# Kernel optimization log

Measured on AMD Instinct MI355X. Metric: run time of the kernel, lower is better.

Reference implementation:

```python
import jax, jax.numpy as jnp
import numpy as np

B, T, NB = 8192, 18, 6
EH, DH = 256, 256
NIN = NB + 1  # encoder GRU input: bits + feedback scalar


def gru_cell(x, h, Wih, Whh, bih, bhh):
    # PyTorch GRU cell: gates ordered (r, z, n)
    gi = x @ Wih.T + bih
    gh = h @ Whh.T + bhh
    ir, iz, inn = jnp.split(gi, 3, axis=-1)
    hr, hz, hn = jnp.split(gh, 3, axis=-1)
    r = jax.nn.sigmoid(ir + hr)
    z = jax.nn.sigmoid(iz + hz)
    n = jnp.tanh(inn + r * hn)
    return (1.0 - z) * n + z * h


def run_gru_dir(seq, Wih, Whh, bih, bhh, reverse):
    # seq: [T, B, D] -> hidden outputs [T, B, H] (aligned to original time order)
    Bn, H = seq.shape[1], Whh.shape[1]
    def step(h, x):
        h2 = gru_cell(x, h, Wih, Whh, bih, bhh)
        return h2, h2
    _, outs = jax.lax.scan(step, jnp.zeros((Bn, H), seq.dtype), seq, reverse=reverse)
    return outs


def setup_inputs() -> dict:
    key = jax.random.key(0)
    ks = jax.random.split(key, 40)
    def w(k, shape, fan):
        s = 1.0 / np.sqrt(fan)
        return jax.random.uniform(k, shape, jnp.float32, -s, s)
    inp = {}
    inp['b'] = (jax.random.uniform(ks[0], (B, NB)) < 0.5).astype(jnp.float32)
    inp['noise1'] = jax.random.normal(ks[1], (B, T, 1), jnp.float32)
    inp['noise2'] = jax.random.normal(ks[2], (B, T, 1), jnp.float32)
    # encoder GRU (2 layers, unidirectional)
    inp['enc_Wih0'] = w(ks[3], (3 * EH, NIN), EH); inp['enc_Whh0'] = w(ks[4], (3 * EH, EH), EH)
    inp['enc_bih0'] = w(ks[5], (3 * EH,), EH);     inp['enc_bhh0'] = w(ks[6], (3 * EH,), EH)
    inp['enc_Wih1'] = w(ks[7], (3 * EH, EH), EH);  inp['enc_Whh1'] = w(ks[8], (3 * EH, EH), EH)
    inp['enc_bih1'] = w(ks[9], (3 * EH,), EH);     inp['enc_bhh1'] = w(ks[10], (3 * EH,), EH)
    inp['enc_lin_W'] = w(ks[11], (1, EH), EH);     inp['enc_lin_b'] = w(ks[12], (1,), EH)
    inp['weight_power'] = jnp.ones((T,), jnp.float32)
    # decoder GRU (2 layers, bidirectional)
    inp['dec_Wih0f'] = w(ks[13], (3 * DH, 1), DH);      inp['dec_Whh0f'] = w(ks[14], (3 * DH, DH), DH)
    inp['dec_bih0f'] = w(ks[15], (3 * DH,), DH);        inp['dec_bhh0f'] = w(ks[16], (3 * DH,), DH)
    inp['dec_Wih0b'] = w(ks[17], (3 * DH, 1), DH);      inp['dec_Whh0b'] = w(ks[18], (3 * DH, DH), DH)
    inp['dec_bih0b'] = w(ks[19], (3 * DH,), DH);        inp['dec_bhh0b'] = w(ks[20], (3 * DH,), DH)
    inp['dec_Wih1f'] = w(ks[21], (3 * DH, 2 * DH), DH); inp['dec_Whh1f'] = w(ks[22], (3 * DH, DH), DH)
    inp['dec_bih1f'] = w(ks[23], (3 * DH,), DH);        inp['dec_bhh1f'] = w(ks[24], (3 * DH,), DH)
    inp['dec_Wih1b'] = w(ks[25], (3 * DH, 2 * DH), DH); inp['dec_Whh1b'] = w(ks[26], (3 * DH, DH), DH)
    inp['dec_bih1b'] = w(ks[27], (3 * DH,), DH);        inp['dec_bhh1b'] = w(ks[28], (3 * DH,), DH)
    inp['dec_lin_W'] = w(ks[29], (NB, 2 * DH), 2 * DH); inp['dec_lin_b'] = w(ks[30], (NB,), 2 * DH)
    inp['weight_merge'] = jnp.ones((T, 2), jnp.float32)
    return inp


def reference(b, noise1, noise2,
              enc_Wih0, enc_Whh0, enc_bih0, enc_bhh0,
              enc_Wih1, enc_Whh1, enc_bih1, enc_bhh1,
              enc_lin_W, enc_lin_b, weight_power,
              dec_Wih0f, dec_Whh0f, dec_bih0f, dec_bhh0f,
              dec_Wih0b, dec_Whh0b, dec_bih0b, dec_bhh0b,
              dec_Wih1f, dec_Whh1f, dec_bih1f, dec_bhh1f,
              dec_Wih1b, dec_Whh1b, dec_bih1b, dec_bhh1b,
              dec_lin_W, dec_lin_b, weight_merge):
    Bn = b.shape[0]
    Tn = weight_power.shape[0]
    # power-normalized per-step weights: sqrt(w^2 * T / sum(w^2))
    wp = jnp.sqrt(weight_power ** 2 * Tn / jnp.sum(weight_power ** 2))

    def enc_step(carry, xs):
        h0, h1, z = carry
        n1, n2, wpt = xs
        inp = jnp.concatenate([b, z], axis=1)            # [B, NB+1]
        h0n = gru_cell(inp, h0, enc_Wih0, enc_Whh0, enc_bih0, enc_bhh0)
        h1n = gru_cell(h0n, h1, enc_Wih1, enc_Whh1, enc_bih1, enc_bhh1)
        xt = jnp.tanh(h1n @ enc_lin_W.T + enc_lin_b)     # [B, 1]
        xn = (xt - jnp.mean(xt)) / jnp.std(xt, ddof=1)   # training-mode batch norm over whole tensor
        y = xn * wpt + n1                                # received symbol
        return (h0n, h1n, y + n2), y                     # feedback z = y + noise2

    carry0 = (jnp.zeros((Bn, EH), b.dtype), jnp.zeros((Bn, EH), b.dtype), jnp.zeros((Bn, 1), b.dtype))
    xs = (jnp.swapaxes(noise1, 0, 1), jnp.swapaxes(noise2, 0, 1), wp)
    _, y_seq = jax.lax.scan(enc_step, carry0, xs)        # [T, B, 1]

    # bidirectional 2-layer decoder GRU over y
    o0f = run_gru_dir(y_seq, dec_Wih0f, dec_Whh0f, dec_bih0f, dec_bhh0f, False)
    o0b = run_gru_dir(y_seq, dec_Wih0b, dec_Whh0b, dec_bih0b, dec_bhh0b, True)
    s1 = jnp.concatenate([o0f, o0b], axis=-1)            # [T, B, 2*DH]
    o1f = run_gru_dir(s1, dec_Wih1f, dec_Whh1f, dec_bih1f, dec_bhh1f, False)
    o1b = run_gru_dir(s1, dec_Wih1b, dec_Whh1b, dec_bih1b, dec_bhh1b, True)

    # attention_type == 5: learned weighted merge over time, per direction
    wf = jnp.sqrt(weight_merge[:, 0] ** 2 * Tn / jnp.sum(weight_merge[:, 0] ** 2))
    wb = jnp.sqrt(weight_merge[:, 1] ** 2 * Tn / jnp.sum(weight_merge[:, 1] ** 2))
    rf = jnp.einsum('tbh,t->bh', o1f, wf)
    rb = jnp.einsum('tbh,t->bh', o1b, wb)
    rc = jnp.concatenate([rf, rb], axis=1)               # [B, 2*DH]
    out = jax.nn.sigmoid(rc @ dec_lin_W.T + dec_lin_b)   # bit_vector output -> sigmoid
    return out.reshape(Bn, -1, 1)
```

## Files before the change

kernel.cpp:

```cpp
#include <hip/hip_runtime.h>
#include <hip/hip_bf16.h>
#include <math.h>

#define BN_ 8192
#define TT 18
#define NBITS 6
#define HH 256
#define G3 768

typedef __hip_bfloat16 hbf16;
typedef __bf16 bf16x8 __attribute__((ext_vector_type(8)));
typedef float f32x4 __attribute__((ext_vector_type(4)));

__device__ inline float sigm(float x){ return 1.0f/(1.0f + expf(-x)); }
__device__ inline float ldx(const void* p, int i, int bf){
    if(bf){ unsigned short u = ((const unsigned short*)p)[i]; return __uint_as_float(((unsigned)u)<<16); }
    return ((const float*)p)[i];
}
__device__ inline __bf16 f2b(float f){ hbf16 h = __float2bfloat16(f); return *reinterpret_cast<__bf16*>(&h); }
__device__ inline float b2f(__bf16 b){ unsigned short u = *reinterpret_cast<unsigned short*>(&b); return __uint_as_float(((unsigned)u)<<16); }
__device__ inline unsigned pack2(float a, float b){
    hbf16 lo = __float2bfloat16(a), hi = __float2bfloat16(b);
    return (unsigned)*(unsigned short*)&lo | ((unsigned)*(unsigned short*)&hi << 16);
}

__global__ __launch_bounds__(256) void fillz(float* __restrict__ p, int n){
    for(int i = blockIdx.x*256 + threadIdx.x; i < n; i += gridDim.x*256) p[i] = 0.0f;
}
__global__ __launch_bounds__(256) void fillb(__bf16* __restrict__ p, int n){
    for(int i = blockIdx.x*256 + threadIdx.x; i < n; i += gridDim.x*256) p[i] = f2b(0.0f);
}

__global__ void prep_w(const void* wp, const void* wm, unsigned* flag,
                       float* wpn, float* wfn, float* wbn){
    if(threadIdx.x==0 && blockIdx.x==0){
        unsigned w0 = *(const unsigned*)wp;
        int bf = ((w0 >> 16) == (w0 & 0xFFFFu)) ? 1 : 0;
        flag[0] = (unsigned)bf;
        float s=0; for(int t=0;t<TT;t++){ float v=ldx(wp,t,bf); s += v*v; }
        for(int t=0;t<TT;t++){ float v=ldx(wp,t,bf); wpn[t] = sqrtf(v*v*TT/s); }
        float sf=0, sb=0;
        for(int t=0;t<TT;t++){ float f=ldx(wm,2*t,bf), b=ldx(wm,2*t+1,bf); sf += f*f; sb += b*b; }
        for(int t=0;t<TT;t++){
            float f=ldx(wm,2*t,bf), b=ldx(wm,2*t+1,bf);
            wfn[t] = sqrtf(f*f*TT/sf);
            wbn[t] = sqrtf(b*b*TT/sb);
        }
    }
}

struct CJ { const void* src; void* dst; int n; int K; int mode; };
struct CJs { CJ j[18]; };
__global__ __launch_bounds__(256) void conv_all(CJs J, const unsigned* __restrict__ flagp){
    const int bf = (int)*flagp;
    CJ c = J.j[blockIdx.y];
    for(int i = blockIdx.x*256 + threadIdx.x; i < c.n; i += gridDim.x*256){
        if(c.mode){
            int row = i / c.K, k = i - row*c.K;
            int g = row>>8, jj = row&255;
            int prow = ((jj>>4)*48) + g*16 + (jj&15);
            ((__bf16*)c.dst)[(size_t)prow*c.K + k] = f2b(ldx(c.src, i, bf));
        }else{
            ((float*)c.dst)[i] = ldx(c.src, i, bf);
        }
    }
}

struct FQ {
    const __bf16* A1; const __bf16* W1; int K1;
    const __bf16* A2; const __bf16* W2; int K2;
    const float* bgi; const float* bgh;
    const __bf16* h; __bf16* hout;
    const void* bits; const void* wih0raw; const void* bih0raw; const float* zf;
    const void* linw; float* xt;
    const float* y; const void* wihraw; const void* bihraw; __bf16* s1t;
    float* racc; const float* wct;
};
struct FQ2 { FQ q[2]; };

template<int MODE>
__global__ __launch_bounds__(256,3) void fused_step(FQ2 PP, const unsigned* __restrict__ flagp){
    const FQ P = PP.q[blockIdx.z];
    const int bf = (int)*flagp;
    __shared__ __align__(16) char smem[28672];
    __bf16* As = (__bf16*)smem;
    __bf16* Ws = (__bf16*)(smem + 16384);
    float*  T  = (float*)smem;
    const int tid = threadIdx.x;
    const int mt = blockIdx.x*8 + (blockIdx.y>>3);
    const int jt = blockIdx.y & 7;
    const int m0 = mt*128;
    const int n0 = jt*96;
    const int lane = tid&63, wv = tid>>6;
    const int wrow = wv>>1, wcol = wv&1;
    const int q = lane>>4, n15 = lane&15;

    f32x4 accR[4], accZ[4], accN1[4], accN2[4];
    #pragma unroll
    for(int i=0;i<4;i++){ accR[i]=(f32x4){0,0,0,0}; accZ[i]=(f32x4){0,0,0,0};
                          accN1[i]=(f32x4){0,0,0,0}; accN2[i]=(f32x4){0,0,0,0}; }

    #pragma unroll
    for(int ph = 0; ph < 2; ph++){
        if(ph==0 && !(MODE==1 || MODE==3)) continue;
        const __bf16* __restrict__ A = ph ? P.A2 : P.A1;
        const __bf16* __restrict__ W = ph ? P.W2 : P.W1;
        const int K = ph ? P.K2 : P.K1;
        for(int k0=0;k0<K;k0+=64){
            #pragma unroll
            for(int s=0;s<4;s++){
                int c = tid + 256*s;
                int row = c>>3, qc = c&7, col = qc ^ ((row>>1)&7);
                *(uint4*)&As[row*64 + col*8] = *(const uint4*)(A + (size_t)(m0+row)*K + k0 + qc*8);
            }
            #pragma unroll
            for(int s=0;s<3;s++){
                int c = tid + 256*s;
                int row = c>>3, qc = c&7, col = qc ^ ((row>>1)&7);
                *(uint4*)&Ws[row*64 + col*8] = *(const uint4*)(W + (size_t)(n0+row)*K + k0 + qc*8);
            }
            __syncthreads();
            #pragma unroll
            for(int ks=0;ks<2;ks++){
                const int cq = ks*4 + q;
                bf16x8 af[4], bfr[3];
                #pragma unroll
                for(int i=0;i<4;i++){
                    int R = wrow*64+i*16+n15;
                    int col = cq ^ ((R>>1)&7);
                    af[i] = *(const bf16x8*)&As[R*64 + col*8];
                }
                #pragma unroll
                for(int g=0;g<3;g++){
                    int RW = wcol*48+g*16+n15;
                    int col = cq ^ ((RW>>1)&7);
                    bfr[g] = *(const bf16x8*)&Ws[RW*64 + col*8];
                }
                #pragma unroll
                for(int i=0;i<4;i++){
                    accR[i] = __builtin_amdgcn_mfma_f32_16x16x32_bf16(af[i], bfr[0], accR[i], 0,0,0);
                    accZ[i] = __builtin_amdgcn_mfma_f32_16x16x32_bf16(af[i], bfr[1], accZ[i], 0,0,0);
                    if(ph) accN2[i] = __builtin_amdgcn_mfma_f32_16x16x32_bf16(af[i], bfr[2], accN2[i], 0,0,0);
                    else   accN1[i] = __builtin_amdgcn_mfma_f32_16x16x32_bf16(af[i], bfr[2], accN1[i], 0,0,0);
                }
            }
            __syncthreads();
        }
    }

    const int jl = wcol*16 + n15;
    const int j  = jt*32 + jl;
    const float bghr = P.bgh[j], bghz = P.bgh[256+j], bghn = P.bgh[512+j];
    float bgir=0, bgiz=0, bgin=0;
    if(MODE==1 || MODE==3){ bgir = P.bgi[j]; bgiz = P.bgi[256+j]; bgin = P.bgi[512+j]; }
    float w0r[7], w0z[7], w0n[7];
    if(MODE==0){
        #pragma unroll
        for(int k=0;k<7;k++){
            w0r[k] = ldx(P.wih0raw, (j    )*7+k, bf);
            w0z[k] = ldx(P.wih0raw, (j+256)*7+k, bf);
            w0n[k] = ldx(P.wih0raw, (j+512)*7+k, bf);
        }
        bgir = ldx(P.bih0raw, j, bf); bgiz = ldx(P.bih0raw, j+256, bf); bgin = ldx(P.bih0raw, j+512, bf);
    }
    float wy_r=0, wy_z=0, wy_n=0;
    if(MODE==2){
        wy_r = ldx(P.wihraw, j, bf); wy_z = ldx(P.wihraw, j+256, bf); wy_n = ldx(P.wihraw, j+512, bf);
        bgir = ldx(P.bihraw, j, bf); bgiz = ldx(P.bihraw, j+256, bf); bgin = ldx(P.bihraw, j+512, bf);
    }
    const float linwj = (MODE==1) ? ldx(P.linw, j, bf) : 0.0f;
    const float wct   = (MODE==3) ? P.wct[0] : 0.0f;

    #pragma unroll
    for(int i=0;i<4;i++){
        const int rbl = wrow*64 + i*16 + q*4;
        float vred[4];
        #pragma unroll
        for(int r=0;r<4;r++){
            const int row_l = rbl + r;
            const int row = m0 + row_l;
            float gir, giz, gin;
            if(MODE==1 || MODE==3){
                gir = bgir; giz = bgiz; gin = accN1[i][r] + bgin;
            }else if(MODE==0){
                gir = bgir; giz = bgiz; gin = bgin;
                #pragma unroll
                for(int k=0;k<NBITS;k++){
                    float bv = ldx(P.bits, row*NBITS+k, bf);
                    gir += bv*w0r[k]; giz += bv*w0z[k]; gin += bv*w0n[k];
                }
                float zb = P.zf[row];
                gir += zb*w0r[6]; giz += zb*w0z[6]; gin += zb*w0n[6];
            }else{
                float yv = P.y[row];
                gir = yv*wy_r + bgir; giz = yv*wy_z + bgiz; gin = yv*wy_n + bgin;
            }
            float rr = sigm(gir + accR[i][r] + bghr);
            float zz = sigm(giz + accZ[i][r] + bghz);
            float nn = tanhf(gin + rr*(accN2[i][r] + bghn));
            float hold = b2f(P.h[(size_t)row*HH + j]);
            float hn = (1.0f - zz)*nn + zz*hold;
            T[row_l*33 + jl] = hn;
            if(MODE==1) vred[r] = hn*linwj;
        }
        if(MODE==1){
            #pragma unroll
            for(int r=0;r<4;r++){
                float v = vred[r];
                #pragma unroll
                for(int m=1;m<16;m<<=1) v += __shfl_xor(v, m);
                if(n15==0) atomicAdd(&P.xt[m0+rbl+r], v);
            }
        }
    }
    __syncthreads();

    const int rw = tid>>2, cw = tid&3;
    #pragma unroll
    for(int pass=0; pass<2; pass++){
        const int row_l = pass*64 + rw;
        const int row = m0 + row_l;
        float v[8];
        #pragma unroll
        for(int u=0;u<8;u++) v[u] = T[row_l*33 + cw*8 + u];
        uint4 pkv = { pack2(v[0],v[1]), pack2(v[2],v[3]), pack2(v[4],v[5]), pack2(v[6],v[7]) };
        *(uint4*)&P.hout[(size_t)row*HH + jt*32 + cw*8] = pkv;
        if(MODE==2) *(uint4*)&P.s1t[(size_t)row*512 + jt*32 + cw*8] = pkv;
        if(MODE==3){
            float* rp = &P.racc[(size_t)row*HH + jt*32 + cw*8];
            float4 a0 = *(float4*)rp, a1 = *(float4*)(rp+4);
            a0.x += wct*v[0]; a0.y += wct*v[1]; a0.z += wct*v[2]; a0.w += wct*v[3];
            a1.x += wct*v[4]; a1.y += wct*v[5]; a1.z += wct*v[6]; a1.w += wct*v[7];
            *(float4*)rp = a0; *(float4*)(rp+4) = a1;
        }
    }
}

__global__ __launch_bounds__(1024) void stats_emit(float* __restrict__ xt, const void* __restrict__ lb,
        const float* __restrict__ wpn, int t, const void* __restrict__ n1, const void* __restrict__ n2,
        float* __restrict__ yseq, float* __restrict__ zf, const unsigned* __restrict__ flagp){
    const int bf = (int)*flagp;
    const float lbv = ldx(lb, 0, bf);
    int tid = threadIdx.x;
    float s=0.0f, ss=0.0f;
    for(int i=tid;i<BN_;i+=1024){ float v = tanhf(xt[i] + lbv); s += v; ss += v*v; }
    #pragma unroll
    for(int o=32;o;o>>=1){ s += __shfl_down(s,o); ss += __shfl_down(ss,o); }
    __shared__ float S[16], SS[16], stm[2];
    if((tid&63)==0){ S[tid>>6]=s; SS[tid>>6]=ss; }
    __syncthreads();
    if(tid==0){
        float a=0.0f, b=0.0f;
        for(int i=0;i<16;i++){ a+=S[i]; b+=SS[i]; }
        float mean = a/(float)BN_;
        float var = (b - (float)BN_*mean*mean)/(float)(BN_-1);
        stm[0]=mean; stm[1]=1.0f/sqrtf(var);
    }
    __syncthreads();
    const float mean=stm[0], rs=stm[1], wt=wpn[t];
    for(int i=tid;i<BN_;i+=1024){
        float v = tanhf(xt[i] + lbv);
        float y = (v-mean)*rs*wt + ldx(n1, i*TT+t, bf);
        yseq[(size_t)t*BN_ + i] = y;
        zf[i] = y + ldx(n2, i*TT+t, bf);
        xt[i] = 0.0f;
    }
}

__global__ __launch_bounds__(256) void final_k(const float* __restrict__ rf, const float* __restrict__ rb,
        const void* __restrict__ W, const void* __restrict__ bias, void* __restrict__ out,
        const unsigned* __restrict__ flagp){
    const int bf = (int)*flagp;
    int lane = threadIdx.x & 63;
    int row = blockIdx.x*4 + (threadIdx.x>>6);
    float a[6] = {};
    #pragma unroll
    for(int i=0;i<4;i++){
        int c = lane + 64*i;
        float xf = rf[(size_t)row*HH + c];
        float xb = rb[(size_t)row*HH + c];
        #pragma unroll
        for(int k=0;k<6;k++) a[k] += xf*ldx(W, k*512 + c, bf) + xb*ldx(W, k*512 + 256 + c, bf);
    }
    #pragma unroll
    for(int o=32;o;o>>=1){
        #pragma unroll
        for(int k=0;k<6;k++) a[k] += __shfl_down(a[k], o);
    }
    if(lane==0){
        #pragma unroll
        for(int k=0;k<6;k++){
            float v = sigm(a[k] + ldx(bias,k,bf));
            if(bf) ((hbf16*)out)[(size_t)row*6+k] = __float2bfloat16(v);
            else   ((float*)out)[(size_t)row*6+k] = v;
        }
    }
}

extern "C" void kernel_launch(void* const* d_in, const int* in_sizes, int n_in,
                              void* d_out, int out_size, void* d_ws, size_t ws_size,
                              hipStream_t stream)
{
    (void)in_sizes; (void)n_in; (void)out_size;
    const void* bits  = d_in[0];
    const void* n1    = d_in[1];
    const void* n2    = d_in[2];
    const void* eWih0 = d_in[3];
    const void* eWhh0 = d_in[4];
    const void* ebih0 = d_in[5];
    const void* ebhh0 = d_in[6];
    const void* eWih1 = d_in[7];
    const void* eWhh1 = d_in[8];
    const void* ebih1 = d_in[9];
    const void* ebhh1 = d_in[10];
    const void* elinW = d_in[11];
    const void* elinb = d_in[12];
    const void* wpow  = d_in[13];
    const void* dWih0f= d_in[14];
    const void* dWhh0f= d_in[15];
    const void* dbih0f= d_in[16];
    const void* dbhh0f= d_in[17];
    const void* dWih0b= d_in[18];
    const void* dWhh0b= d_in[19];
    const void* dbih0b= d_in[20];
    const void* dbhh0b= d_in[21];
    const void* dWih1f= d_in[22];
    const void* dWhh1f= d_in[23];
    const void* dbih1f= d_in[24];
    const void* dbhh1f= d_in[25];
    const void* dWih1b= d_in[26];
    const void* dWhh1b= d_in[27];
    const void* dbih1b= d_in[28];
    const void* dbhh1b= d_in[29];
    const void* dlinW = d_in[30];
    const void* dlinb = d_in[31];
    const void* wmrg  = d_in[32];

    float* base = (float*)d_ws;
    size_t off = 0;
    auto alloc  = [&](size_t n){ float* p = base + off; off += (n + 63) & ~(size_t)63; return p; };
    auto allocb = [&](size_t n){ __bf16* p = (__bf16*)(base + off); off += ((n/2) + 63) & ~(size_t)63; return p; };
    unsigned* flag = (unsigned*)alloc(64);
    float* wpn = alloc(TT); float* wfn = alloc(TT); float* wbn = alloc(TT);
    const int WK = HH*G3;
    __bf16* WeHH0 = allocb(WK);  __bf16* WeIH1 = allocb(WK);  __bf16* WeHH1 = allocb(WK);
    __bf16* Wd0f  = allocb(WK);  __bf16* Wd0b  = allocb(WK);
    __bf16* Wd1fI = allocb(2*WK);__bf16* Wd1bI = allocb(2*WK);
    __bf16* Wd1fH = allocb(WK);  __bf16* Wd1bH = allocb(WK);
    float* BeHH0 = alloc(G3); float* BeIH1 = alloc(G3); float* BeHH1 = alloc(G3);
    float* Bd0f  = alloc(G3); float* Bd0b  = alloc(G3);
    float* Bd1fI = alloc(G3); float* Bd1bI = alloc(G3);
    float* Bd1fH = alloc(G3); float* Bd1bH = alloc(G3);
    const size_t NH = (size_t)BN_*HH;
    __bf16* X0 = allocb(NH);  __bf16* X1 = allocb(NH);
    __bf16* Y0 = allocb(NH);  __bf16* Y1 = allocb(NH);
    float* rf  = alloc(NH);
    float* rb  = alloc(NH);
    float* xt  = alloc(BN_);
    float* zf  = alloc(BN_);
    float* yseq= alloc((size_t)TT*BN_);
    __bf16* s1 = allocb((size_t)TT*BN_*512);
    size_t need = off*sizeof(float);
    if(ws_size < need) return;

    prep_w<<<1,64,0,stream>>>(wpow, wmrg, flag, wpn, wfn, wbn);
    CJs J;
    const void* ws_src[18] = {eWhh0,eWih1,eWhh1,dWhh0f,dWhh0b,dWih1f,dWih1b,dWhh1f,dWhh1b,
                              ebhh0,ebih1,ebhh1,dbhh0f,dbhh0b,dbih1f,dbih1b,dbhh1f,dbhh1b};
    void* ws_dst[18] = {WeHH0,WeIH1,WeHH1,Wd0f,Wd0b,Wd1fI,Wd1bI,Wd1fH,Wd1bH,
                        BeHH0,BeIH1,BeHH1,Bd0f,Bd0b,Bd1fI,Bd1bI,Bd1fH,Bd1bH};
    int ws_n[18] = {WK,WK,WK,WK,WK,2*WK,2*WK,WK,WK, G3,G3,G3,G3,G3,G3,G3,G3,G3};
    int ws_K[18] = {256,256,256,256,256,512,512,256,256, 0,0,0,0,0,0,0,0,0};
    for(int i=0;i<18;i++){ J.j[i] = {ws_src[i], ws_dst[i], ws_n[i], ws_K[i], (i<9)?1:0}; }
    conv_all<<<dim3(768,18),256,0,stream>>>(J, flag);
    fillb<<<1024,256,0,stream>>>(X0, (int)NH);
    fillb<<<1024,256,0,stream>>>(Y0, (int)NH);
    fillz<<<32,256,0,stream>>>(xt, BN_);
    fillz<<<32,256,0,stream>>>(zf, BN_);

    dim3 g1(8, 64, 1), g2(8, 64, 2);
    __bf16* X[2] = {X0, X1};
    __bf16* Y[2] = {Y0, Y1};

    int p = 0;
    for(int t=0;t<TT;t++){
        FQ2 P0{}; FQ2 P1{};
        P0.q[0] = {nullptr,nullptr,0, X[p],WeHH0,HH, nullptr,BeHH0, X[p],X[1-p],
                   bits,eWih0,ebih0,zf, nullptr,nullptr, nullptr,nullptr,nullptr,nullptr, nullptr,nullptr};
        fused_step<0><<<g1,256,0,stream>>>(P0, flag);
        P1.q[0] = {X[1-p],WeIH1,HH, Y[p],WeHH1,HH, BeIH1,BeHH1, Y[p],Y[1-p],
                   nullptr,nullptr,nullptr,nullptr, elinW,xt, nullptr,nullptr,nullptr,nullptr, nullptr,nullptr};
        fused_step<1><<<g1,256,0,stream>>>(P1, flag);
        stats_emit<<<1,1024,0,stream>>>(xt, elinb, wpn, t, n1, n2, yseq, zf, flag);
        p ^= 1;
    }

    fillb<<<1024,256,0,stream>>>(X0, (int)NH);
    fillb<<<1024,256,0,stream>>>(Y0, (int)NH);
    p = 0;
    for(int i=0;i<TT;i++){
        int tf = i, tb = TT-1-i;
        FQ2 P{};
        P.q[0] = {nullptr,nullptr,0, X[p],Wd0f,HH, nullptr,Bd0f, X[p],X[1-p],
                  nullptr,nullptr,nullptr,nullptr, nullptr,nullptr,
                  yseq+(size_t)tf*BN_, dWih0f, dbih0f, s1+(size_t)tf*BN_*512, nullptr,nullptr};
        P.q[1] = {nullptr,nullptr,0, Y[p],Wd0b,HH, nullptr,Bd0b, Y[p],Y[1-p],
                  nullptr,nullptr,nullptr,nullptr, nullptr,nullptr,
                  yseq+(size_t)tb*BN_, dWih0b, dbih0b, s1+(size_t)tb*BN_*512+256, nullptr,nullptr};
        fused_step<2><<<g2,256,0,stream>>>(P, flag);
        p ^= 1;
    }

    fillb<<<1024,256,0,stream>>>(X0, (int)NH);
    fillb<<<1024,256,0,stream>>>(Y0, (int)NH);
    fillz<<<1024,256,0,stream>>>(rf, (int)(2*NH));
    p = 0;
    for(int i=0;i<TT;i++){
        int tf = i, tb = TT-1-i;
        FQ2 P{};
        P.q[0] = {s1+(size_t)tf*BN_*512, Wd1fI, 512, X[p],Wd1fH,HH, Bd1fI,Bd1fH, X[p],X[1-p],
                  nullptr,nullptr,nullptr,nullptr, nullptr,nullptr, nullptr,nullptr,nullptr,nullptr,
                  rf, wfn+tf};
        P.q[1] = {s1+(size_t)tb*BN_*512, Wd1bI, 512, Y[p],Wd1bH,HH, Bd1bI,Bd1bH, Y[p],Y[1-p],
                  nullptr,nullptr,nullptr,nullptr, nullptr,nullptr, nullptr,nullptr,nullptr,nullptr,
                  rb, wbn+tb};
        fused_step<3><<<g2,256,0,stream>>>(P, flag);
        p ^= 1;
    }

    final_k<<<BN_/4,256,0,stream>>>(rf, rb, dlinW, dlinb, d_out, flag);
}
```

Measured before the change: 2.023 ms.

## Fuse encoder stats into last-block of GRU step and use direct-to-LDS loads

After: 3.178 ms. 57.1% more time.

```diff
diff --git a/kernel.cpp b/kernel.cpp
--- a/kernel.cpp
+++ b/kernel.cpp
@@ -22,6 +22,10 @@
 __device__ inline unsigned pack2(float a, float b){
     hbf16 lo = __float2bfloat16(a), hi = __float2bfloat16(b);
     return (unsigned)*(unsigned short*)&lo | ((unsigned)*(unsigned short*)&hi << 16);
+}
+__device__ inline void gload16(const void* g, void* l){
+    __builtin_amdgcn_global_load_lds((const __attribute__((address_space(1))) void*)g,
+                                     (__attribute__((address_space(3))) void*)l, 16, 0, 0);
 }
 
 __global__ __launch_bounds__(256) void fillz(float* __restrict__ p, int n){
@@ -50,16 +54,19 @@
 }
 
 struct CJ { const void* src; void* dst; int n; int K; int mode; };
-struct CJs { CJ j[18]; };
+struct CJs { CJ j[20]; };
 __global__ __launch_bounds__(256) void conv_all(CJs J, const unsigned* __restrict__ flagp){
     const int bf = (int)*flagp;
     CJ c = J.j[blockIdx.y];
     for(int i = blockIdx.x*256 + threadIdx.x; i < c.n; i += gridDim.x*256){
-        if(c.mode){
+        if(c.mode==1){
             int row = i / c.K, k = i - row*c.K;
             int g = row>>8, jj = row&255;
             int prow = ((jj>>4)*48) + g*16 + (jj&15);
             ((__bf16*)c.dst)[(size_t)prow*c.K + k] = f2b(ldx(c.src, i, bf));
+        }else if(c.mode==2){
+            int t = i >> 13, b = i & (BN_-1);
+            ((float*)c.dst)[i] = ldx(c.src, b*TT + t, bf);
         }else{
             ((float*)c.dst)[i] = ldx(c.src, i, bf);
         }
@@ -72,7 +79,8 @@
     const float* bgi; const float* bgh;
     const __bf16* h; __bf16* hout;
     const void* bits; const void* wih0raw; const void* bih0raw; const float* zf;
-    const void* linw; float* xt;
+    const void* linw; float* xt; unsigned* cnt; const void* lb;
+    const float* wpt; const float* n1t; const float* n2t; float* ys; float* zfo;
     const float* y; const void* wihraw; const void* bihraw; __bf16* s1t;
     float* racc; const float* wct;
 };
@@ -94,6 +102,8 @@
     const int lane = tid&63, wv = tid>>6;
     const int wrow = wv>>1, wcol = wv&1;
     const int q = lane>>4, n15 = lane&15;
+    const int rA = wv*8 + (lane>>3);
+    const int qc = lane&7;
 
     f32x4 accR[4], accZ[4], accN1[4], accN2[4];
     #pragma unroll
@@ -109,15 +119,15 @@
         for(int k0=0;k0<K;k0+=64){
             #pragma unroll
             for(int s=0;s<4;s++){
-                int c = tid + 256*s;
-                int row = c>>3, qc = c&7, col = qc ^ ((row>>1)&7);
-                *(uint4*)&As[row*64 + col*8] = *(const uint4*)(A + (size_t)(m0+row)*K + k0 + qc*8);
+                int row = s*32 + rA;
+                int sc = (row>>1)&7;
+                gload16(A + (size_t)(m0+row)*K + k0 + ((qc^sc)<<3), As + (size_t)(s*32 + wv*8)*64);
             }
             #pragma unroll
             for(int s=0;s<3;s++){
-                int c = tid + 256*s;
-                int row = c>>3, qc = c&7, col = qc ^ ((row>>1)&7);
-                *(uint4*)&Ws[row*64 + col*8] = *(const uint4*)(W + (size_t)(n0+row)*K + k0 + qc*8);
+                int row = s*32 + rA;
+                int sc = (row>>1)&7;
+                gload16(W + (size_t)(n0+row)*K + k0 + ((qc^sc)<<3), Ws + (size_t)(s*32 + wv*8)*64);
             }
             __syncthreads();
             #pragma unroll
@@ -234,36 +244,41 @@
             *(float4*)rp = a0; *(float4*)(rp+4) = a1;
         }
     }
-}
-
-__global__ __launch_bounds__(1024) void stats_emit(float* __restrict__ xt, const void* __restrict__ lb,
-        const float* __restrict__ wpn, int t, const void* __restrict__ n1, const void* __restrict__ n2,
-        float* __restrict__ yseq, float* __restrict__ zf, const unsigned* __restrict__ flagp){
-    const int bf = (int)*flagp;
-    const float lbv = ldx(lb, 0, bf);
-    int tid = threadIdx.x;
-    float s=0.0f, ss=0.0f;
-    for(int i=tid;i<BN_;i+=1024){ float v = tanhf(xt[i] + lbv); s += v; ss += v*v; }
-    #pragma unroll
-    for(int o=32;o;o>>=1){ s += __shfl_down(s,o); ss += __shfl_down(ss,o); }
-    __shared__ float S[16], SS[16], stm[2];
-    if((tid&63)==0){ S[tid>>6]=s; SS[tid>>6]=ss; }
-    __syncthreads();
-    if(tid==0){
-        float a=0.0f, b=0.0f;
-        for(int i=0;i<16;i++){ a+=S[i]; b+=SS[i]; }
-        float mean = a/(float)BN_;
-        float var = (b - (float)BN_*mean*mean)/(float)(BN_-1);
-        stm[0]=mean; stm[1]=1.0f/sqrtf(var);
-    }
-    __syncthreads();
-    const float mean=stm[0], rs=stm[1], wt=wpn[t];
-    for(int i=tid;i<BN_;i+=1024){
-        float v = tanhf(xt[i] + lbv);
-        float y = (v-mean)*rs*wt + ldx(n1, i*TT+t, bf);
-        yseq[(size_t)t*BN_ + i] = y;
-        zf[i] = y + ldx(n2, i*TT+t, bf);
-        xt[i] = 0.0f;
+
+    if(MODE==1){
+        __shared__ unsigned done;
+        __threadfence();
+        if(tid==0) done = (atomicAdd(P.cnt, 1u) == 511u) ? 1u : 0u;
+        __syncthreads();
+        if(done){
+            const float lbv = ldx(P.lb, 0, bf);
+            float s=0.0f, ss=0.0f;
+            for(int i2=tid;i2<BN_;i2+=256){
+                float xv = __hip_atomic_load(&P.xt[i2], __ATOMIC_RELAXED, __HIP_MEMORY_SCOPE_AGENT);
+                float v = tanhf(xv + lbv); s += v; ss += v*v;
+            }
+            #pragma unroll
+            for(int o=32;o;o>>=1){ s += __shfl_down(s,o); ss += __shfl_down(ss,o); }
+            __shared__ float RS[8], stm[2];
+            if((tid&63)==0){ RS[tid>>6]=s; RS[4+(tid>>6)]=ss; }
+            __syncthreads();
+            if(tid==0){
+                float a=RS[0]+RS[1]+RS[2]+RS[3], b2=RS[4]+RS[5]+RS[6]+RS[7];
+                float mean = a/(float)BN_;
+                float var = (b2 - (float)BN_*mean*mean)/(float)(BN_-1);
+                stm[0]=mean; stm[1]=1.0f/sqrtf(var);
+            }
+            __syncthreads();
+            const float mean=stm[0], rs=stm[1], wt=P.wpt[0];
+            for(int i2=tid;i2<BN_;i2+=256){
+                float xv = __hip_atomic_load(&P.xt[i2], __ATOMIC_RELAXED, __HIP_MEMORY_SCOPE_AGENT);
+                float v = tanhf(xv + lbv);
+                float yv = (v-mean)*rs*wt + P.n1t[i2];
+                P.ys[i2] = yv;
+                P.zfo[i2] = yv + P.n2t[i2];
+                P.xt[i2] = 0.0f;
+            }
+        }
     }
 }
 
@@ -357,25 +372,29 @@
     float* rf  = alloc(NH);
     float* rb  = alloc(NH);
     float* xt  = alloc(BN_);
+    unsigned* cnts = (unsigned*)alloc(64);
     float* zf  = alloc(BN_);
     float* yseq= alloc((size_t)TT*BN_);
+    float* n1t = alloc((size_t)TT*BN_);
+    float* n2t = alloc((size_t)TT*BN_);
     __bf16* s1 = allocb((size_t)TT*BN_*512);
     size_t need = off*sizeof(float);
     if(ws_size < need) return;
 
     prep_w<<<1,64,0,stream>>>(wpow, wmrg, flag, wpn, wfn, wbn);
     CJs J;
-    const void* ws_src[18] = {eWhh0,eWih1,eWhh1,dWhh0f,dWhh0b,dWih1f,dWih1b,dWhh1f,dWhh1b,
-                              ebhh0,ebih1,ebhh1,dbhh0f,dbhh0b,dbih1f,dbih1b,dbhh1f,dbhh1b};
-    void* ws_dst[18] = {WeHH0,WeIH1,WeHH1,Wd0f,Wd0b,Wd1fI,Wd1bI,Wd1fH,Wd1bH,
-                        BeHH0,BeIH1,BeHH1,Bd0f,Bd0b,Bd1fI,Bd1bI,Bd1fH,Bd1bH};
-    int ws_n[18] = {WK,WK,WK,WK,WK,2*WK,2*WK,WK,WK, G3,G3,G3,G3,G3,G3,G3,G3,G3};
-    int ws_K[18] = {256,256,256,256,256,512,512,256,256, 0,0,0,0,0,0,0,0,0};
-    for(int i=0;i<18;i++){ J.j[i] = {ws_src[i], ws_dst[i], ws_n[i], ws_K[i], (i<9)?1:0}; }
-    conv_all<<<dim3(768,18),256,0,stream>>>(J, flag);
+    const void* ws_src[20] = {eWhh0,eWih1,eWhh1,dWhh0f,dWhh0b,dWih1f,dWih1b,dWhh1f,dWhh1b,
+                              ebhh0,ebih1,ebhh1,dbhh0f,dbhh0b,dbih1f,dbih1b,dbhh1f,dbhh1b, n1, n2};
+    void* ws_dst[20] = {WeHH0,WeIH1,WeHH1,Wd0f,Wd0b,Wd1fI,Wd1bI,Wd1fH,Wd1bH,
+                        BeHH0,BeIH1,BeHH1,Bd0f,Bd0b,Bd1fI,Bd1bI,Bd1fH,Bd1bH, n1t, n2t};
+    int ws_n[20] = {WK,WK,WK,WK,WK,2*WK,2*WK,WK,WK, G3,G3,G3,G3,G3,G3,G3,G3,G3, TT*BN_, TT*BN_};
+    int ws_K[20] = {256,256,256,256,256,512,512,256,256, 0,0,0,0,0,0,0,0,0, 0,0};
+    int ws_m[20] = {1,1,1,1,1,1,1,1,1, 0,0,0,0,0,0,0,0,0, 2,2};
+    for(int i=0;i<20;i++){ J.j[i] = {ws_src[i], ws_dst[i], ws_n[i], ws_K[i], ws_m[i]}; }
+    conv_all<<<dim3(768,20),256,0,stream>>>(J, flag);
     fillb<<<1024,256,0,stream>>>(X0, (int)NH);
     fillb<<<1024,256,0,stream>>>(Y0, (int)NH);
-    fillz<<<32,256,0,stream>>>(xt, BN_);
+    fillz<<<32,256,0,stream>>>(xt, BN_+64);
     fillz<<<32,256,0,stream>>>(zf, BN_);
 
     dim3 g1(8, 64, 1), g2(8, 64, 2);
@@ -385,13 +404,17 @@
     int p = 0;
     for(int t=0;t<TT;t++){
         FQ2 P0{}; FQ2 P1{};
-        P0.q[0] = {nullptr,nullptr,0, X[p],WeHH0,HH, nullptr,BeHH0, X[p],X[1-p],
-                   bits,eWih0,ebih0,zf, nullptr,nullptr, nullptr,nullptr,nullptr,nullptr, nullptr,nullptr};
+        FQ& a = P0.q[0];
+        a.A2=X[p]; a.W2=WeHH0; a.K2=HH; a.bgh=BeHH0; a.h=X[p]; a.hout=X[1-p];
+        a.bits=bits; a.wih0raw=eWih0; a.bih0raw=ebih0; a.zf=zf;
         fused_step<0><<<g1,256,0,stream>>>(P0, flag);
-        P1.q[0] = {X[1-p],WeIH1,HH, Y[p],WeHH1,HH, BeIH1,BeHH1, Y[p],Y[1-p],
-                   nullptr,nullptr,nullptr,nullptr, elinW,xt, nullptr,nullptr,nullptr,nullptr, nullptr,nullptr};
+        FQ& b = P1.q[0];
+        b.A1=X[1-p]; b.W1=WeIH1; b.K1=HH; b.A2=Y[p]; b.W2=WeHH1; b.K2=HH;
+        b.bgi=BeIH1; b.bgh=BeHH1; b.h=Y[p]; b.hout=Y[1-p];
+        b.linw=elinW; b.xt=xt; b.cnt=cnts+t; b.lb=elinb;
+        b.wpt=wpn+t; b.n1t=n1t+(size_t)t*BN_; b.n2t=n2t+(size_t)t*BN_;
+        b.ys=yseq+(size_t)t*BN_; b.zfo=zf;
         fused_step<1><<<g1,256,0,stream>>>(P1, flag);
-        stats_emit<<<1,1024,0,stream>>>(xt, elinb, wpn, t, n1, n2, yseq, zf, flag);
         p ^= 1;
     }
 
@@ -401,12 +424,12 @@
     for(int i=0;i<TT;i++){
         int tf = i, tb = TT-1-i;
         FQ2 P{};
-        P.q[0] = {nullptr,nullptr,0, X[p],Wd0f,HH, nullptr,Bd0f, X[p],X[1-p],
-                  nullptr,nullptr,nullptr,nullptr, nullptr,nullptr,
-                  yseq+(size_t)tf*BN_, dWih0f, dbih0f, s1+(size_t)tf*BN_*512, nullptr,nullptr};
-        P.q[1] = {nullptr,nullptr,0, Y[p],Wd0b,HH, nullptr,Bd0b, Y[p],Y[1-p],
-                  nullptr,nullptr,nullptr,nullptr, nullptr,nullptr,
-                  yseq+(size_t)tb*BN_, dWih0b, dbih0b, s1+(size_t)tb*BN_*512+256, nullptr,nullptr};
+        FQ& a = P.q[0];
+        a.A2=X[p]; a.W2=Wd0f; a.K2=HH; a.bgh=Bd0f; a.h=X[p]; a.hout=X[1-p];
+        a.y=yseq+(size_t)tf*BN_; a.wihraw=dWih0f; a.bihraw=dbih0f; a.s1t=s1+(size_t)tf*BN_*512;
+        FQ& b = P.q[1];
+        b.A2=Y[p]; b.W2=Wd0b; b.K2=HH; b.bgh=Bd0b; b.h=Y[p]; b.hout=Y[1-p];
+        b.y=yseq+(size_t)tb*BN_; b.wihraw=dWih0b; b.bihraw=dbih0b; b.s1t=s1+(size_t)tb*BN_*512+256;
         fused_step<2><<<g2,256,0,stream>>>(P, flag);
         p ^= 1;
     }
@@ -418,12 +441,14 @@
     for(int i=0;i<TT;i++){
         int tf = i, tb = TT-1-i;
         FQ2 P{};
-        P.q[0] = {s1+(size_t)tf*BN_*512, Wd1fI, 512, X[p],Wd1fH,HH, Bd1fI,Bd1fH, X[p],X[1-p],
-                  nullptr,nullptr,nullptr,nullptr, nullptr,nullptr, nullptr,nullptr,nullptr,nullptr,
-                  rf, wfn+tf};
-        P.q[1] = {s1+(size_t)tb*BN_*512, Wd1bI, 512, Y[p],Wd1bH,HH, Bd1bI,Bd1bH, Y[p],Y[1-p],
-                  nullptr,nullptr,nullptr,nullptr, nullptr,nullptr, nullptr,nullptr,nullptr,nullptr,
-                  rb, wbn+tb};
+        FQ& a = P.q[0];
+        a.A1=s1+(size_t)tf*BN_*512; a.W1=Wd1fI; a.K1=512;
+        a.A2=X[p]; a.W2=Wd1fH; a.K2=HH; a.bgi=Bd1fI; a.bgh=Bd1fH; a.h=X[p]; a.hout=X[1-p];
+        a.racc=rf; a.wct=wfn+tf;
+        FQ& b = P.q[1];
+        b.A1=s1+(size_t)tb*BN_*512; b.W1=Wd1bI; b.K1=512;
+        b.A2=Y[p]; b.W2=Wd1bH; b.K2=HH; b.bgi=Bd1bI; b.bgh=Bd1bH; b.h=Y[p]; b.hout=Y[1-p];
+        b.racc=rb; b.wct=wbn+tb;
         fused_step<3><<<g2,256,0,stream>>>(P, flag);
         p ^= 1;
     }
```
